# Kernel tuning notes

Hardware: AMD Instinct MI355X
Metric: run time of the kernel (lower is better)

The kernel has to match this reference:

```python
import jax, jax.numpy as jnp
import numpy as np

BS, NQ, DIM, HEADS, POINTS, LEVELS = 2, 4096, 768, 6, 4, 1
HD = DIM // HEADS
H = W = 64
NV = H * W
EPS = 1e-6


def setup_inputs() -> dict:
    key = jax.random.key(0)
    ks = jax.random.split(key, 16)
    s = 0.02  # param init scale
    return {
        "query": jax.random.normal(ks[0], (BS, NQ, DIM), jnp.float32),
        "reference_points": jax.random.uniform(ks[1], (BS, NQ, LEVELS, 2), jnp.float32),
        "feat": jax.random.normal(ks[2], (BS, NV, DIM), jnp.float32),
        "spatial_shapes": np.array([[H, W]], dtype=np.int64),
        "level_start_index": np.array([0], dtype=np.int64),
        "ln_w": jnp.ones((DIM,), jnp.float32),
        "ln_b": jnp.zeros((DIM,), jnp.float32),
        "vp_w": jax.random.normal(ks[3], (DIM, DIM), jnp.float32) * s,
        "vp_b": jnp.zeros((DIM,), jnp.float32),
        "off_w": jax.random.normal(ks[4], (DIM, HEADS * LEVELS * POINTS * 2), jnp.float32) * s,
        "off_b": jax.random.normal(ks[5], (HEADS * LEVELS * POINTS * 2,), jnp.float32),
        "aw_w": jax.random.normal(ks[6], (DIM, HEADS * LEVELS * POINTS), jnp.float32) * s,
        "aw_b": jnp.zeros((HEADS * LEVELS * POINTS,), jnp.float32),
        "out_w": jax.random.normal(ks[7], (DIM, DIM), jnp.float32) * s,
        "out_b": jnp.zeros((DIM,), jnp.float32),
        "gamma": jax.random.normal(ks[8], (DIM,), jnp.float32) * 0.1,
    }


def _layernorm(x, w, b):
    mu = jnp.mean(x, axis=-1, keepdims=True)
    var = jnp.mean(jnp.square(x - mu), axis=-1, keepdims=True)
    return (x - mu) * jax.lax.rsqrt(var + EPS) * w + b


def _bilinear_sample(img, loc):
    # img: (bs, heads, H, W, hd); loc: (bs, nq, heads, points, 2) in [0,1]
    # matches torch.grid_sample(align_corners=False, padding_mode='zeros')
    bs, heads, h, w, hd = img.shape
    x = loc[..., 0] * w - 0.5
    y = loc[..., 1] * h - 0.5
    x0 = jnp.floor(x)
    y0 = jnp.floor(y)
    wx = x - x0
    wy = y - y0
    x0i = x0.astype(jnp.int32)
    y0i = y0.astype(jnp.int32)
    bi = jnp.arange(bs)[:, None, None, None]
    hi = jnp.arange(heads)[None, None, :, None]

    def gather(yi, xi):
        valid = (xi >= 0) & (xi < w) & (yi >= 0) & (yi < h)
        v = img[bi, hi, jnp.clip(yi, 0, h - 1), jnp.clip(xi, 0, w - 1)]
        return v * valid[..., None].astype(img.dtype)

    v00 = gather(y0i, x0i)
    v01 = gather(y0i, x0i + 1)
    v10 = gather(y0i + 1, x0i)
    v11 = gather(y0i + 1, x0i + 1)
    wx = wx[..., None]
    wy = wy[..., None]
    return (v00 * (1 - wy) * (1 - wx) + v01 * (1 - wy) * wx
            + v10 * wy * (1 - wx) + v11 * wy * wx)


def _msda(q, value, reference_points, spatial_shapes, off_w, off_b, aw_w, aw_b, out_w, out_b):
    bs, nq, _ = q.shape
    nv = value.shape[1]
    value = value.reshape(bs, nv, HEADS, HD)
    offsets = (q @ off_w + off_b).reshape(bs, nq, HEADS, LEVELS, POINTS, 2)
    aw = jax.nn.softmax(q @ aw_w + aw_b, axis=-1).reshape(bs, nq, HEADS, LEVELS, POINTS)
    # offset_normalizer = [W_l, H_l] per level
    norm = jnp.asarray(np.asarray(spatial_shapes)[:, ::-1], jnp.float32)  # (L, 2)
    loc = reference_points[:, :, None, :, None, :] + offsets / norm[None, None, None, :, None, :]
    # loc: (bs, nq, heads, levels, points, 2)
    out = jnp.zeros((bs, nq, HEADS, HD), jnp.float32)
    start = 0
    for l in range(LEVELS):
        h_l, w_l = int(spatial_shapes[l][0]), int(spatial_shapes[l][1])
        img = value[:, start:start + h_l * w_l].reshape(bs, h_l, w_l, HEADS, HD).transpose(0, 3, 1, 2, 4)
        sampled = _bilinear_sample(img, loc[:, :, :, l])  # (bs, nq, heads, points, hd)
        out = out + jnp.einsum('bnhpd,bnhp->bnhd', sampled, aw[:, :, :, l])
        start += h_l * w_l
    return out.reshape(bs, nq, DIM) @ out_w + out_b


def reference(query, reference_points, feat, spatial_shapes, level_start_index,
              ln_w, ln_b, vp_w, vp_b, off_w, off_b, aw_w, aw_b, out_w, out_b, gamma):
    q = _layernorm(query, ln_w, ln_b)
    value = feat @ vp_w + vp_b
    attn = _msda(q, value, reference_points, spatial_shapes,
                 off_w, off_b, aw_w, aw_b, out_w, out_b)
    # identity = zeros, dropout = 0 -> attn as-is; residual scale by gamma
    return query + gamma * attn
```

## Files before the change

### kernel.cpp

```cpp
#include <hip/hip_runtime.h>
#include <hip/hip_bf16.h>
#include <math.h>

#define BSZ 2
#define NQ 4096
#define DIM 768
#define HEADS 6
#define POINTS 4
#define HD 128
#define HW_DIM 64
#define NV (HW_DIM*HW_DIM)
#define M_TOTAL (BSZ*NQ)
#define KDIM 768
#define KSPLIT 4
#define KPART (KDIM/KSPLIT)

#define BM 64
#define BN 128
#define BKK 64
#define NBLK_M (M_TOTAL/BM)
#define NBLK_N (DIM/BN)
#define GEMM_GRID (NBLK_M*NBLK_N)

typedef __attribute__((ext_vector_type(8))) short bf16x8;
typedef __attribute__((ext_vector_type(4))) float f32x4;
typedef unsigned int u32;
typedef unsigned short u16;

__device__ inline u16 f2bf(float f) {
    union { float f; u32 u; } v; v.f = f;
    u32 r = v.u + 0x7fffu + ((v.u >> 16) & 1u);
    return (u16)(r >> 16);
}

#define GLD16(g, l) __builtin_amdgcn_global_load_lds( \
    (const __attribute__((address_space(1))) u32*)(g), \
    (__attribute__((address_space(3))) u32*)(l), 16, 0, 0)

__global__ __launch_bounds__(256) void ln_bf_kernel(const float* __restrict__ x,
        const float* __restrict__ w, const float* __restrict__ b,
        u16* __restrict__ q) {
    int wave = threadIdx.x >> 6, lane = threadIdx.x & 63;
    int row = blockIdx.x * 4 + wave;
    int c = lane * 4;
    const float* xr = x + (size_t)row * DIM;
    float4 v0 = *(const float4*)(xr + c);
    float4 v1 = *(const float4*)(xr + c + 256);
    float4 v2 = *(const float4*)(xr + c + 512);
    float s  = v0.x+v0.y+v0.z+v0.w + v1.x+v1.y+v1.z+v1.w + v2.x+v2.y+v2.z+v2.w;
    float ss = v0.x*v0.x+v0.y*v0.y+v0.z*v0.z+v0.w*v0.w
             + v1.x*v1.x+v1.y*v1.y+v1.z*v1.z+v1.w*v1.w
             + v2.x*v2.x+v2.y*v2.y+v2.z*v2.z+v2.w*v2.w;
    #pragma unroll
    for (int st = 1; st < 64; st <<= 1) {
        s  += __shfl_xor(s,  st, 64);
        ss += __shfl_xor(ss, st, 64);
    }
    float mean = s * (1.0f / DIM);
    float var  = ss * (1.0f / DIM) - mean * mean;
    float rstd = rsqrtf(var + 1e-6f);
    u16* qr = q + (size_t)row * DIM;
    #pragma unroll
    for (int g = 0; g < 3; g++) {
        float4 v = (g == 0) ? v0 : (g == 1) ? v1 : v2;
        int cc = c + g * 256;
        const float4 ww = *(const float4*)(w + cc);
        const float4 bb = *(const float4*)(b + cc);
        ushort4 o;
        o.x = f2bf((v.x - mean) * rstd * ww.x + bb.x);
        o.y = f2bf((v.y - mean) * rstd * ww.y + bb.y);
        o.z = f2bf((v.z - mean) * rstd * ww.z + bb.z);
        o.w = f2bf((v.w - mean) * rstd * ww.w + bb.w);
        *(ushort4*)(qr + cc) = o;
    }
}

__global__ __launch_bounds__(256) void transpose_all(
        const float* __restrict__ vp_w,  u16* __restrict__ vp_wt,
        const float* __restrict__ out_w, u16* __restrict__ out_wt,
        const float* __restrict__ off_w, const float* __restrict__ aw_w,
        u16* __restrict__ oaw_wt) {
    int z = blockIdx.z;
    if (z == 2 && blockIdx.x >= 3) return;
    __shared__ float tile[32][33];
    int n0 = blockIdx.x * 32, k0 = blockIdx.y * 32;
    int tx = threadIdx.x & 31, ty = threadIdx.x >> 5;
    const float* src = (z == 0) ? vp_w : (z == 1) ? out_w : nullptr;
    u16* dst = (z == 0) ? vp_wt : (z == 1) ? out_wt : oaw_wt;
    #pragma unroll
    for (int r = 0; r < 4; r++) {
        int k = k0 + ty + r * 8, n = n0 + tx;
        float v = 0.0f;
        if (z < 2) {
            v = src[(size_t)k * DIM + n];
        } else {
            if (n < 48) v = off_w[(size_t)k * 48 + n];
            else if (n < 72) v = aw_w[(size_t)k * 24 + (n - 48)];
        }
        tile[ty + r * 8][tx] = v;
    }
    __syncthreads();
    #pragma unroll
    for (int r = 0; r < 4; r++) {
        int nn = ty + r * 8, kk = tx;
        int drow = n0 + nn;
        if (z == 2 && drow >= 80) continue;
        dst[(size_t)drow * KDIM + k0 + kk] = f2bf(tile[kk][nn]);
    }
}

template<int AFP32>
__global__ __launch_bounds__(256, 3) void gemm_bt(
        const void* __restrict__ Avoid, const u16* __restrict__ Bt,
        const float* __restrict__ bias, void* __restrict__ Cout,
        int storeBF16, const float* __restrict__ resid,
        const float* __restrict__ gamma) {
    __shared__ u16 As[BM * BKK];
    __shared__ u16 Bs[BN * BKK];
    int tid = threadIdx.x, w = tid >> 6, lane = tid & 63;
    int lm = lane & 15, quad = lane >> 4;
    int b = blockIdx.x;
    int xcd = b & 7, idx = b >> 3;
    int mb = xcd * 16 + idx / NBLK_N;
    int nb = idx % NBLK_N;
    int m0 = mb * BM, n0 = nb * BN;
    int wr = w & 1, wc = w >> 1;

    int srow = lane >> 3;
    int scol = (lane & 7) ^ srow;
    const u16* Bb = Bt + (size_t)n0 * KDIM;
    const u16* Ab16 = (const u16*)Avoid + (size_t)m0 * KDIM;
    const float* Ab32 = (const float*)Avoid + (size_t)m0 * KDIM;
    int arow = tid >> 2, acb0 = (tid & 3) * 2;

    f32x4 acc[2][4];
    #pragma unroll
    for (int i = 0; i < 2; i++)
        #pragma unroll
        for (int j = 0; j < 4; j++) acc[i][j] = (f32x4){0.f, 0.f, 0.f, 0.f};

    const u16* aaddr[2][2];
    const u16* baddr[4][2];
    #pragma unroll
    for (int i = 0; i < 2; i++) {
        int row = wr * 32 + i * 16 + lm;
        #pragma unroll
        for (int kk = 0; kk < 2; kk++)
            aaddr[i][kk] = &As[row * BKK + (((quad + 4 * kk) ^ (row & 7)) << 3)];
    }
    #pragma unroll
    for (int j = 0; j < 4; j++) {
        int row = wc * 64 + j * 16 + lm;
        #pragma unroll
        for (int kk = 0; kk < 2; kk++)
            baddr[j][kk] = &Bs[row * BKK + (((quad + 4 * kk) ^ (row & 7)) << 3)];
    }

    for (int k0 = 0; k0 < KDIM; k0 += BKK) {
        if (AFP32) {
            const float* ag = Ab32 + (size_t)arow * KDIM + k0 + acb0 * 8;
            float4 f0 = *(const float4*)ag;
            float4 f1 = *(const float4*)(ag + 4);
            float4 f2 = *(const float4*)(ag + 8);
            float4 f3 = *(const float4*)(ag + 12);
            bf16x8 p0, p1;
            p0[0]=f2bf(f0.x); p0[1]=f2bf(f0.y); p0[2]=f2bf(f0.z); p0[3]=f2bf(f0.w);
            p0[4]=f2bf(f1.x); p0[5]=f2bf(f1.y); p0[6]=f2bf(f1.z); p0[7]=f2bf(f1.w);
            p1[0]=f2bf(f2.x); p1[1]=f2bf(f2.y); p1[2]=f2bf(f2.z); p1[3]=f2bf(f2.w);
            p1[4]=f2bf(f3.x); p1[5]=f2bf(f3.y); p1[6]=f2bf(f3.z); p1[7]=f2bf(f3.w);
            *(bf16x8*)&As[arow * BKK + (((acb0)     ^ (arow & 7)) << 3)] = p0;
            *(bf16x8*)&As[arow * BKK + (((acb0 + 1) ^ (arow & 7)) << 3)] = p1;
        } else {
            #pragma unroll
            for (int r = 0; r < 2; r++) {
                int row = r * 32 + w * 8 + srow;
                GLD16(Ab16 + (size_t)row * KDIM + k0 + scol * 8, &As[(r * 32 + w * 8) * BKK]);
            }
        }
        #pragma unroll
        for (int r = 0; r < 4; r++) {
            int row = r * 32 + w * 8 + srow;
            GLD16(Bb + (size_t)row * KDIM + k0 + scol * 8, &Bs[(r * 32 + w * 8) * BKK]);
        }
        __syncthreads();
        #pragma unroll
        for (int kk = 0; kk < 2; kk++) {
            bf16x8 af[2], bf[4];
            #pragma unroll
            for (int i = 0; i < 2; i++) af[i] = *(const bf16x8*)aaddr[i][kk];
            #pragma unroll
            for (int j = 0; j < 4; j++) bf[j] = *(const bf16x8*)baddr[j][kk];
            #pragma unroll
            for (int i = 0; i < 2; i++)
                #pragma unroll
                for (int j = 0; j < 4; j++)
                    acc[i][j] = __builtin_amdgcn_mfma_f32_16x16x32_bf16(af[i], bf[j], acc[i][j], 0, 0, 0);
        }
        __syncthreads();
    }

    #pragma unroll
    for (int j = 0; j < 4; j++) {
        int col = n0 + wc * 64 + j * 16 + lm;
        float bb = bias[col];
        #pragma unroll
        for (int i = 0; i < 2; i++) {
            #pragma unroll
            for (int r = 0; r < 4; r++) {
                int row = m0 + wr * 32 + i * 16 + quad * 4 + r;
                size_t idxo = (size_t)row * DIM + col;
                float v = acc[i][j][r] + bb;
                if (storeBF16) {
                    ((u16*)Cout)[idxo] = f2bf(v);
                } else {
                    ((float*)Cout)[idxo] = resid[idxo] + gamma[col] * v;
                }
            }
        }
    }
}

__global__ __launch_bounds__(256, 2) void gemm_small(
        const u16* __restrict__ A, const u16* __restrict__ Bt,
        const float* __restrict__ b0, const float* __restrict__ b1,
        float* __restrict__ C, int M, int K) {
    __shared__ u16 As[64 * 32];
    __shared__ u16 Bs[80 * 32];
    int tid = threadIdx.x, wave = tid >> 6, lane = tid & 63;
    int lm = lane & 15, quad = lane >> 4;
    int m0 = blockIdx.x * 64;
    int part = blockIdx.y;
    int kbase = part * KPART;
    f32x4 acc[5];
    #pragma unroll
    for (int i = 0; i < 5; i++) acc[i] = (f32x4){0.f, 0.f, 0.f, 0.f};
    int lrow = lane >> 2, lcol = (lane & 3) * 8;

    for (int k0 = kbase; k0 < kbase + KPART; k0 += 32) {
        for (int c = wave; c < 9; c += 4) {
            if (c < 4) {
                GLD16(A + (size_t)(m0 + c * 16 + lrow) * K + k0 + lcol, &As[c * 16 * 32]);
            } else {
                GLD16(Bt + (size_t)((c - 4) * 16 + lrow) * K + k0 + lcol, &Bs[(c - 4) * 16 * 32]);
            }
        }
        __syncthreads();
        bf16x8 af = *(const bf16x8*)&As[(wave * 16 + lm) * 32 + quad * 8];
        #pragma unroll
        for (int bn = 0; bn < 5; bn++) {
            bf16x8 bv = *(const bf16x8*)&Bs[(bn * 16 + lm) * 32 + quad * 8];
            acc[bn] = __builtin_amdgcn_mfma_f32_16x16x32_bf16(af, bv, acc[bn], 0, 0, 0);
        }
        __syncthreads();
    }
    float* Cp = C + (size_t)part * M_TOTAL * 80;
    #pragma unroll
    for (int bn = 0; bn < 5; bn++) {
        int col = bn * 16 + lm;
        float bb = 0.0f;
        if (part == 0) bb = (col < 48) ? b0[col] : ((col < 72) ? b1[col - 48] : 0.0f);
        #pragma unroll
        for (int r = 0; r < 4; r++) {
            int row = m0 + wave * 16 + quad * 4 + r;
            Cp[(size_t)row * 80 + col] = acc[bn][r] + bb;
        }
    }
}

__global__ __launch_bounds__(384) void sample_kernel(
        const float* __restrict__ oa, const float* __restrict__ refp,
        const u16* __restrict__ v, u16* __restrict__ out) {
    int row = blockIdx.x;
    int b = row >> 12;
    int tid = threadIdx.x;
    __shared__ float s_w[4][24];
    __shared__ int   s_o[4][24];
    __shared__ float s_e[24];
    if (tid < 24) {
        int h = tid >> 2, p = tid & 3;
        float ox = 0.f, oy = 0.f, lg = 0.f;
        #pragma unroll
        for (int part = 0; part < KSPLIT; part++) {
            const float* pp = oa + (size_t)part * M_TOTAL * 80 + (size_t)row * 80;
            ox += pp[h * 8 + p * 2 + 0];
            oy += pp[h * 8 + p * 2 + 1];
            lg += pp[48 + tid];
        }
        float rx = refp[row * 2 + 0], ry = refp[row * 2 + 1];
        float x = (rx + ox * (1.0f / HW_DIM)) * HW_DIM - 0.5f;
        float y = (ry + oy * (1.0f / HW_DIM)) * HW_DIM - 0.5f;
        float fx = floorf(x), fy = floorf(y);
        int x0 = (int)fx, y0 = (int)fy;
        int x1 = x0 + 1, y1 = y0 + 1;
        float wx = x - fx, wy = y - fy;
        float vx0 = (x0 >= 0 && x0 < HW_DIM) ? 1.f : 0.f;
        float vx1 = (x1 >= 0 && x1 < HW_DIM) ? 1.f : 0.f;
        float vy0 = (y0 >= 0 && y0 < HW_DIM) ? 1.f : 0.f;
        float vy1 = (y1 >= 0 && y1 < HW_DIM) ? 1.f : 0.f;
        int xc0 = min(max(x0, 0), HW_DIM - 1), xc1 = min(max(x1, 0), HW_DIM - 1);
        int yc0 = min(max(y0, 0), HW_DIM - 1), yc1 = min(max(y1, 0), HW_DIM - 1);
        int base = b * NV * DIM;
        s_o[0][tid] = base + (yc0 * HW_DIM + xc0) * DIM;
        s_o[1][tid] = base + (yc0 * HW_DIM + xc1) * DIM;
        s_o[2][tid] = base + (yc1 * HW_DIM + xc0) * DIM;
        s_o[3][tid] = base + (yc1 * HW_DIM + xc1) * DIM;
        s_w[0][tid] = (1.f - wy) * (1.f - wx) * vy0 * vx0;
        s_w[1][tid] = (1.f - wy) * wx * vy0 * vx1;
        s_w[2][tid] = wy * (1.f - wx) * vy1 * vx0;
        s_w[3][tid] = wy * wx * vy1 * vx1;
        s_e[tid] = lg;
        float m = s_e[0];
        #pragma unroll
        for (int i = 1; i < 24; i++) m = fmaxf(m, s_e[i]);
        s_e[tid] = expf(lg - m);
    }
    __syncthreads();
    float ssum = 0.0f;
    #pragma unroll
    for (int i = 0; i < 24; i++) ssum += s_e[i];
    float inv = 1.0f / ssum;

    int h = tid >> 6;
    int d2 = (tid & 63) * 2;
    const u16* vb = v + h * HD + d2;
    float a0 = 0.0f, a1 = 0.0f;
    #pragma unroll
    for (int p = 0; p < 4; p++) {
        int idx = h * 4 + p;
        float aw = s_e[idx] * inv;
        #pragma unroll
        for (int c = 0; c < 4; c++) {
            u32 u = *(const u32*)(vb + s_o[c][idx]);
            float w = aw * s_w[c][idx];
            a0 += w * __uint_as_float(u << 16);
            a1 += w * __uint_as_float(u & 0xffff0000u);
        }
    }
    u32 pack = (u32)f2bf(a0) | ((u32)f2bf(a1) << 16);
    *(u32*)&out[(size_t)row * DIM + h * HD + d2] = pack;
}

extern "C" void kernel_launch(void* const* d_in, const int* in_sizes, int n_in,
                              void* d_out, int out_size, void* d_ws, size_t ws_size,
                              hipStream_t stream) {
    const float* query = (const float*)d_in[0];
    const float* refp  = (const float*)d_in[1];
    const float* feat  = (const float*)d_in[2];
    const float* ln_w  = (const float*)d_in[5];
    const float* ln_b  = (const float*)d_in[6];
    const float* vp_w  = (const float*)d_in[7];
    const float* vp_b  = (const float*)d_in[8];
    const float* off_w = (const float*)d_in[9];
    const float* off_b = (const float*)d_in[10];
    const float* aw_w  = (const float*)d_in[11];
    const float* aw_b  = (const float*)d_in[12];
    const float* out_w = (const float*)d_in[13];
    const float* out_b = (const float*)d_in[14];
    const float* gamma = (const float*)d_in[15];

    const size_t MD = (size_t)M_TOTAL * DIM;
    char* ws = (char*)d_ws;
    u16* q_bf    = (u16*)ws;                 ws += MD * 2;
    u16* v_bf    = (u16*)ws;                 ws += MD * 2;
    u16* s_bf    = (u16*)ws;                 ws += MD * 2;
    u16* vp_wt   = (u16*)ws;                 ws += (size_t)DIM * DIM * 2;
    u16* out_wt  = (u16*)ws;                 ws += (size_t)DIM * DIM * 2;
    u16* oaw_wt  = (u16*)ws;                 ws += (size_t)80 * KDIM * 2;
    float* oa    = (float*)ws;               ws += (size_t)KSPLIT * M_TOTAL * 80 * 4;
    float* out_f = (float*)d_out;

    ln_bf_kernel<<<M_TOTAL / 4, 256, 0, stream>>>(query, ln_w, ln_b, q_bf);
    transpose_all<<<dim3(24, 24, 3), 256, 0, stream>>>(vp_w, vp_wt, out_w, out_wt,
                                                       off_w, aw_w, oaw_wt);
    gemm_bt<1><<<GEMM_GRID, 256, 0, stream>>>(feat, vp_wt, vp_b, v_bf,
                                              1, nullptr, nullptr);
    gemm_small<<<dim3(128, KSPLIT), 256, 0, stream>>>(q_bf, oaw_wt, off_b, aw_b, oa, M_TOTAL, KDIM);
    sample_kernel<<<M_TOTAL, 384, 0, stream>>>(oa, refp, v_bf, s_bf);
    gemm_bt<0><<<GEMM_GRID, 256, 0, stream>>>(s_bf, out_wt, out_b, out_f,
                                              0, query, gamma);
}
```

Baseline: 200.7 us.

## Merge prep kernels and co-launch value-projection and offset GEMMs

```diff
diff --git a/kernel.cpp b/kernel.cpp
--- a/kernel.cpp
+++ b/kernel.cpp
@@ -21,6 +21,8 @@
 #define NBLK_M (M_TOTAL/BM)
 #define NBLK_N (DIM/BN)
 #define GEMM_GRID (NBLK_M*NBLK_N)
+#define LN_BLOCKS (M_TOTAL/4)
+#define TR_BLOCKS (576+576+72)
 
 typedef __attribute__((ext_vector_type(8))) short bf16x8;
 typedef __attribute__((ext_vector_type(4))) float f32x4;
@@ -37,81 +39,98 @@
     (const __attribute__((address_space(1))) u32*)(g), \
     (__attribute__((address_space(3))) u32*)(l), 16, 0, 0)
 
-__global__ __launch_bounds__(256) void ln_bf_kernel(const float* __restrict__ x,
-        const float* __restrict__ w, const float* __restrict__ b,
-        u16* __restrict__ q) {
-    int wave = threadIdx.x >> 6, lane = threadIdx.x & 63;
-    int row = blockIdx.x * 4 + wave;
-    int c = lane * 4;
-    const float* xr = x + (size_t)row * DIM;
-    float4 v0 = *(const float4*)(xr + c);
-    float4 v1 = *(const float4*)(xr + c + 256);
-    float4 v2 = *(const float4*)(xr + c + 512);
-    float s  = v0.x+v0.y+v0.z+v0.w + v1.x+v1.y+v1.z+v1.w + v2.x+v2.y+v2.z+v2.w;
-    float ss = v0.x*v0.x+v0.y*v0.y+v0.z*v0.z+v0.w*v0.w
-             + v1.x*v1.x+v1.y*v1.y+v1.z*v1.z+v1.w*v1.w
-             + v2.x*v2.x+v2.y*v2.y+v2.z*v2.z+v2.w*v2.w;
-    #pragma unroll
-    for (int st = 1; st < 64; st <<= 1) {
-        s  += __shfl_xor(s,  st, 64);
-        ss += __shfl_xor(ss, st, 64);
-    }
-    float mean = s * (1.0f / DIM);
-    float var  = ss * (1.0f / DIM) - mean * mean;
-    float rstd = rsqrtf(var + 1e-6f);
-    u16* qr = q + (size_t)row * DIM;
-    #pragma unroll
-    for (int g = 0; g < 3; g++) {
-        float4 v = (g == 0) ? v0 : (g == 1) ? v1 : v2;
-        int cc = c + g * 256;
-        const float4 ww = *(const float4*)(w + cc);
-        const float4 bb = *(const float4*)(b + cc);
-        ushort4 o;
-        o.x = f2bf((v.x - mean) * rstd * ww.x + bb.x);
-        o.y = f2bf((v.y - mean) * rstd * ww.y + bb.y);
-        o.z = f2bf((v.z - mean) * rstd * ww.z + bb.z);
-        o.w = f2bf((v.w - mean) * rstd * ww.w + bb.w);
-        *(ushort4*)(qr + cc) = o;
-    }
-}
-
-__global__ __launch_bounds__(256) void transpose_all(
+__global__ __launch_bounds__(256) void prep_kernel(
+        const float* __restrict__ x, const float* __restrict__ lnw,
+        const float* __restrict__ lnb, u16* __restrict__ q,
+        const float* __restrict__ feat, u16* __restrict__ feat_bf,
         const float* __restrict__ vp_w,  u16* __restrict__ vp_wt,
         const float* __restrict__ out_w, u16* __restrict__ out_wt,
         const float* __restrict__ off_w, const float* __restrict__ aw_w,
         u16* __restrict__ oaw_wt) {
-    int z = blockIdx.z;
-    if (z == 2 && blockIdx.x >= 3) return;
-    __shared__ float tile[32][33];
-    int n0 = blockIdx.x * 32, k0 = blockIdx.y * 32;
-    int tx = threadIdx.x & 31, ty = threadIdx.x >> 5;
-    const float* src = (z == 0) ? vp_w : (z == 1) ? out_w : nullptr;
-    u16* dst = (z == 0) ? vp_wt : (z == 1) ? out_wt : oaw_wt;
-    #pragma unroll
-    for (int r = 0; r < 4; r++) {
-        int k = k0 + ty + r * 8, n = n0 + tx;
-        float v = 0.0f;
-        if (z < 2) {
-            v = src[(size_t)k * DIM + n];
-        } else {
-            if (n < 48) v = off_w[(size_t)k * 48 + n];
-            else if (n < 72) v = aw_w[(size_t)k * 24 + (n - 48)];
-        }
-        tile[ty + r * 8][tx] = v;
-    }
-    __syncthreads();
-    #pragma unroll
-    for (int r = 0; r < 4; r++) {
-        int nn = ty + r * 8, kk = tx;
-        int drow = n0 + nn;
-        if (z == 2 && drow >= 80) continue;
-        dst[(size_t)drow * KDIM + k0 + kk] = f2bf(tile[kk][nn]);
-    }
-}
-
-template<int AFP32>
-__global__ __launch_bounds__(256, 3) void gemm_bt(
-        const void* __restrict__ Avoid, const u16* __restrict__ Bt,
+    int b = blockIdx.x;
+    if (b < LN_BLOCKS) {
+        int wave = threadIdx.x >> 6, lane = threadIdx.x & 63;
+        int row = b * 4 + wave;
+        int c = lane * 4;
+        const float* xr = x + (size_t)row * DIM;
+        const float* fr = feat + (size_t)row * DIM;
+        float4 v0 = *(const float4*)(xr + c);
+        float4 v1 = *(const float4*)(xr + c + 256);
+        float4 v2 = *(const float4*)(xr + c + 512);
+        float4 f0 = *(const float4*)(fr + c);
+        float4 f1 = *(const float4*)(fr + c + 256);
+        float4 f2 = *(const float4*)(fr + c + 512);
+        u16* fb = feat_bf + (size_t)row * DIM;
+        ushort4 fo;
+        fo.x = f2bf(f0.x); fo.y = f2bf(f0.y); fo.z = f2bf(f0.z); fo.w = f2bf(f0.w);
+        *(ushort4*)(fb + c) = fo;
+        fo.x = f2bf(f1.x); fo.y = f2bf(f1.y); fo.z = f2bf(f1.z); fo.w = f2bf(f1.w);
+        *(ushort4*)(fb + c + 256) = fo;
+        fo.x = f2bf(f2.x); fo.y = f2bf(f2.y); fo.z = f2bf(f2.z); fo.w = f2bf(f2.w);
+        *(ushort4*)(fb + c + 512) = fo;
+
+        float s  = v0.x+v0.y+v0.z+v0.w + v1.x+v1.y+v1.z+v1.w + v2.x+v2.y+v2.z+v2.w;
+        float ss = v0.x*v0.x+v0.y*v0.y+v0.z*v0.z+v0.w*v0.w
+                 + v1.x*v1.x+v1.y*v1.y+v1.z*v1.z+v1.w*v1.w
+                 + v2.x*v2.x+v2.y*v2.y+v2.z*v2.z+v2.w*v2.w;
+        #pragma unroll
+        for (int st = 1; st < 64; st <<= 1) {
+            s  += __shfl_xor(s,  st, 64);
+            ss += __shfl_xor(ss, st, 64);
+        }
+        float mean = s * (1.0f / DIM);
+        float var  = ss * (1.0f / DIM) - mean * mean;
+        float rstd = rsqrtf(var + 1e-6f);
+        u16* qr = q + (size_t)row * DIM;
+        #pragma unroll
+        for (int g = 0; g < 3; g++) {
+            float4 v = (g == 0) ? v0 : (g == 1) ? v1 : v2;
+            int cc = c + g * 256;
+            const float4 ww = *(const float4*)(lnw + cc);
+            const float4 bb = *(const float4*)(lnb + cc);
+            ushort4 o;
+            o.x = f2bf((v.x - mean) * rstd * ww.x + bb.x);
+            o.y = f2bf((v.y - mean) * rstd * ww.y + bb.y);
+            o.z = f2bf((v.z - mean) * rstd * ww.z + bb.z);
+            o.w = f2bf((v.w - mean) * rstd * ww.w + bb.w);
+            *(ushort4*)(qr + cc) = o;
+        }
+    } else {
+        int t = b - LN_BLOCKS;
+        int z, xk, yk;
+        if (t < 576)      { z = 0; xk = t % 24; yk = t / 24; }
+        else if (t < 1152){ z = 1; t -= 576; xk = t % 24; yk = t / 24; }
+        else              { z = 2; t -= 1152; xk = t % 3; yk = t / 3; }
+        __shared__ float tile[32][33];
+        int n0 = xk * 32, k0 = yk * 32;
+        int tx = threadIdx.x & 31, ty = threadIdx.x >> 5;
+        const float* src = (z == 0) ? vp_w : (z == 1) ? out_w : nullptr;
+        u16* dst = (z == 0) ? vp_wt : (z == 1) ? out_wt : oaw_wt;
+        #pragma unroll
+        for (int r = 0; r < 4; r++) {
+            int k = k0 + ty + r * 8, n = n0 + tx;
+            float v = 0.0f;
+            if (z < 2) {
+                v = src[(size_t)k * DIM + n];
+            } else {
+                if (n < 48) v = off_w[(size_t)k * 48 + n];
+                else if (n < 72) v = aw_w[(size_t)k * 24 + (n - 48)];
+            }
+            tile[ty + r * 8][tx] = v;
+        }
+        __syncthreads();
+        #pragma unroll
+        for (int r = 0; r < 4; r++) {
+            int nn = ty + r * 8, kk = tx;
+            int drow = n0 + nn;
+            if (z == 2 && drow >= 80) continue;
+            dst[(size_t)drow * KDIM + k0 + kk] = f2bf(tile[kk][nn]);
+        }
+    }
+}
+
+__device__ __forceinline__ void gemm_big_body(int b,
+        const u16* __restrict__ A, const u16* __restrict__ Bt,
         const float* __restrict__ bias, void* __restrict__ Cout,
         int storeBF16, const float* __restrict__ resid,
         const float* __restrict__ gamma) {
@@ -119,7 +138,6 @@
     __shared__ u16 Bs[BN * BKK];
     int tid = threadIdx.x, w = tid >> 6, lane = tid & 63;
     int lm = lane & 15, quad = lane >> 4;
-    int b = blockIdx.x;
     int xcd = b & 7, idx = b >> 3;
     int mb = xcd * 16 + idx / NBLK_N;
     int nb = idx % NBLK_N;
@@ -128,10 +146,8 @@
 
     int srow = lane >> 3;
     int scol = (lane & 7) ^ srow;
+    const u16* Ab = A + (size_t)m0 * KDIM;
     const u16* Bb = Bt + (size_t)n0 * KDIM;
-    const u16* Ab16 = (const u16*)Avoid + (size_t)m0 * KDIM;
-    const float* Ab32 = (const float*)Avoid + (size_t)m0 * KDIM;
-    int arow = tid >> 2, acb0 = (tid & 3) * 2;
 
     f32x4 acc[2][4];
     #pragma unroll
@@ -157,25 +173,10 @@
     }
 
     for (int k0 = 0; k0 < KDIM; k0 += BKK) {
-        if (AFP32) {
-            const float* ag = Ab32 + (size_t)arow * KDIM + k0 + acb0 * 8;
-            float4 f0 = *(const float4*)ag;
-            float4 f1 = *(const float4*)(ag + 4);
-            float4 f2 = *(const float4*)(ag + 8);
-            float4 f3 = *(const float4*)(ag + 12);
-            bf16x8 p0, p1;
-            p0[0]=f2bf(f0.x); p0[1]=f2bf(f0.y); p0[2]=f2bf(f0.z); p0[3]=f2bf(f0.w);
-            p0[4]=f2bf(f1.x); p0[5]=f2bf(f1.y); p0[6]=f2bf(f1.z); p0[7]=f2bf(f1.w);
-            p1[0]=f2bf(f2.x); p1[1]=f2bf(f2.y); p1[2]=f2bf(f2.z); p1[3]=f2bf(f2.w);
-            p1[4]=f2bf(f3.x); p1[5]=f2bf(f3.y); p1[6]=f2bf(f3.z); p1[7]=f2bf(f3.w);
-            *(bf16x8*)&As[arow * BKK + (((acb0)     ^ (arow & 7)) << 3)] = p0;
-            *(bf16x8*)&As[arow * BKK + (((acb0 + 1) ^ (arow & 7)) << 3)] = p1;
-        } else {
-            #pragma unroll
-            for (int r = 0; r < 2; r++) {
-                int row = r * 32 + w * 8 + srow;
-                GLD16(Ab16 + (size_t)row * KDIM + k0 + scol * 8, &As[(r * 32 + w * 8) * BKK]);
-            }
+        #pragma unroll
+        for (int r = 0; r < 2; r++) {
+            int row = r * 32 + w * 8 + srow;
+            GLD16(Ab + (size_t)row * KDIM + k0 + scol * 8, &As[(r * 32 + w * 8) * BKK]);
         }
         #pragma unroll
         for (int r = 0; r < 4; r++) {
@@ -220,16 +221,15 @@
     }
 }
 
-__global__ __launch_bounds__(256, 2) void gemm_small(
+__device__ __forceinline__ void gemm_small_body(int mblk, int part,
         const u16* __restrict__ A, const u16* __restrict__ Bt,
         const float* __restrict__ b0, const float* __restrict__ b1,
-        float* __restrict__ C, int M, int K) {
-    __shared__ u16 As[64 * 32];
-    __shared__ u16 Bs[80 * 32];
+        float* __restrict__ C) {
+    __shared__ u16 As2[64 * 32];
+    __shared__ u16 Bs2[80 * 32];
     int tid = threadIdx.x, wave = tid >> 6, lane = tid & 63;
     int lm = lane & 15, quad = lane >> 4;
-    int m0 = blockIdx.x * 64;
-    int part = blockIdx.y;
+    int m0 = mblk * 64;
     int kbase = part * KPART;
     f32x4 acc[5];
     #pragma unroll
@@ -239,16 +239,16 @@
     for (int k0 = kbase; k0 < kbase + KPART; k0 += 32) {
         for (int c = wave; c < 9; c += 4) {
             if (c < 4) {
-                GLD16(A + (size_t)(m0 + c * 16 + lrow) * K + k0 + lcol, &As[c * 16 * 32]);
+                GLD16(A + (size_t)(m0 + c * 16 + lrow) * KDIM + k0 + lcol, &As2[c * 16 * 32]);
             } else {
-                GLD16(Bt + (size_t)((c - 4) * 16 + lrow) * K + k0 + lcol, &Bs[(c - 4) * 16 * 32]);
+                GLD16(Bt + (size_t)((c - 4) * 16 + lrow) * KDIM + k0 + lcol, &Bs2[(c - 4) * 16 * 32]);
             }
         }
         __syncthreads();
-        bf16x8 af = *(const bf16x8*)&As[(wave * 16 + lm) * 32 + quad * 8];
+        bf16x8 af = *(const bf16x8*)&As2[(wave * 16 + lm) * 32 + quad * 8];
         #pragma unroll
         for (int bn = 0; bn < 5; bn++) {
-            bf16x8 bv = *(const bf16x8*)&Bs[(bn * 16 + lm) * 32 + quad * 8];
+            bf16x8 bv = *(const bf16x8*)&Bs2[(bn * 16 + lm) * 32 + quad * 8];
             acc[bn] = __builtin_amdgcn_mfma_f32_16x16x32_bf16(af, bv, acc[bn], 0, 0, 0);
         }
         __syncthreads();
@@ -265,6 +265,28 @@
             Cp[(size_t)row * 80 + col] = acc[bn][r] + bb;
         }
     }
+}
+
+__global__ __launch_bounds__(256, 3) void gemms_kernel(
+        const u16* __restrict__ feat_bf, const u16* __restrict__ vp_wt,
+        const float* __restrict__ vp_b, u16* __restrict__ v_bf,
+        const u16* __restrict__ q_bf, const u16* __restrict__ oaw_wt,
+        const float* __restrict__ off_b, const float* __restrict__ aw_b,
+        float* __restrict__ oa) {
+    int b = blockIdx.x;
+    if (b < GEMM_GRID) {
+        gemm_big_body(b, feat_bf, vp_wt, vp_b, v_bf, 1, nullptr, nullptr);
+    } else {
+        int t = b - GEMM_GRID;
+        gemm_small_body(t & 127, t >> 7, q_bf, oaw_wt, off_b, aw_b, oa);
+    }
+}
+
+__global__ __launch_bounds__(256, 3) void outgemm_kernel(
+        const u16* __restrict__ s_bf, const u16* __restrict__ out_wt,
+        const float* __restrict__ out_b, float* __restrict__ out_f,
+        const float* __restrict__ query, const float* __restrict__ gamma) {
+    gemm_big_body(blockIdx.x, s_bf, out_wt, out_b, out_f, 0, query, gamma);
 }
 
 __global__ __launch_bounds__(384) void sample_kernel(
@@ -361,6 +383,7 @@
     const size_t MD = (size_t)M_TOTAL * DIM;
     char* ws = (char*)d_ws;
     u16* q_bf    = (u16*)ws;                 ws += MD * 2;
+    u16* feat_bf = (u16*)ws;                 ws += MD * 2;
     u16* v_bf    = (u16*)ws;                 ws += MD * 2;
     u16* s_bf    = (u16*)ws;                 ws += MD * 2;
     u16* vp_wt   = (u16*)ws;                 ws += (size_t)DIM * DIM * 2;
@@ -369,13 +392,11 @@
     float* oa    = (float*)ws;               ws += (size_t)KSPLIT * M_TOTAL * 80 * 4;
     float* out_f = (float*)d_out;
 
-    ln_bf_kernel<<<M_TOTAL / 4, 256, 0, stream>>>(query, ln_w, ln_b, q_bf);
-    transpose_all<<<dim3(24, 24, 3), 256, 0, stream>>>(vp_w, vp_wt, out_w, out_wt,
-                                                       off_w, aw_w, oaw_wt);
-    gemm_bt<1><<<GEMM_GRID, 256, 0, stream>>>(feat, vp_wt, vp_b, v_bf,
-                                              1, nullptr, nullptr);
-    gemm_small<<<dim3(128, KSPLIT), 256, 0, stream>>>(q_bf, oaw_wt, off_b, aw_b, oa, M_TOTAL, KDIM);
+    prep_kernel<<<LN_BLOCKS + TR_BLOCKS, 256, 0, stream>>>(
+        query, ln_w, ln_b, q_bf, feat, feat_bf,
+        vp_w, vp_wt, out_w, out_wt, off_w, aw_w, oaw_wt);
+    gemms_kernel<<<GEMM_GRID + 128 * KSPLIT, 256, 0, stream>>>(
+        feat_bf, vp_wt, vp_b, v_bf, q_bf, oaw_wt, off_b, aw_b, oa);
     sample_kernel<<<M_TOTAL, 384, 0, stream>>>(oa, refp, v_bf, s_bf);
-    gemm_bt<0><<<GEMM_GRID, 256, 0, stream>>>(s_bf, out_wt, out_b, out_f,
-                                              0, query, gamma);
-}
+    outgemm_kernel<<<GEMM_GRID, 256, 0, stream>>>(s_bf, out_wt, out_b, out_f, query, gamma);
+}
```

New measurement: 180.7 us. 10.0% less time.
